# Kernel optimization log

Measured on AMD Instinct MI355X. Metric: run time of the kernel, lower is better.

The kernel has to match this reference:

```python
import jax, jax.numpy as jnp
import numpy as np

B, N, D_IN, D, H = 4, 256, 600, 600, 256  # batch, nodes, in_dim, mem_dim, attn hidden


def setup_inputs() -> dict:
    key = jax.random.key(0)
    ks = jax.random.split(key, 12)
    feature = jax.random.normal(ks[0], (B, N, D_IN), dtype=jnp.float32)
    latent_adj = jax.random.randint(ks[1], (B, N, N), 0, 2).astype(jnp.float32)
    s_in = 1.0 / np.sqrt(D_IN)
    s_d = 1.0 / np.sqrt(D)
    s_2d = 1.0 / np.sqrt(2 * D)
    s_h = 1.0 / np.sqrt(H)
    W0 = jax.random.uniform(ks[2], (D_IN, D), jnp.float32, -s_in, s_in)
    b0 = jax.random.uniform(ks[3], (D,), jnp.float32, -s_in, s_in)
    W1 = jax.random.uniform(ks[4], (D, D), jnp.float32, -s_d, s_d)
    b1 = jax.random.uniform(ks[5], (D,), jnp.float32, -s_d, s_d)
    aW1 = jax.random.uniform(ks[6], (2 * D, H), jnp.float32, -s_2d, s_2d)
    ab1 = jax.random.uniform(ks[7], (H,), jnp.float32, -s_2d, s_2d)
    aW2 = jax.random.uniform(ks[8], (H,), jnp.float32, -s_h, s_h)
    ab2 = jax.random.uniform(ks[9], (1,), jnp.float32, -s_h, s_h)
    return {"feature": feature, "latent_adj": latent_adj, "W0": W0, "b0": b0,
            "W1": W1, "b1": b1, "aW1": aW1, "ab1": ab1, "aW2": aW2, "ab2": ab2}


def _gat_layer(x, Wl, bl, aW1, ab1, aW2, ab2, adj):
    h = jnp.einsum('bni,io->bno', x, Wl) + bl                    # [B,N,D]
    # Decompose first attn linear: [h_i, h_j] @ aW1 = h_i @ aW1[:D] + h_j @ aW1[D:]
    left = jnp.einsum('bnd,dh->bnh', h, aW1[:h.shape[-1]])        # i-part
    right = jnp.einsum('bnd,dh->bnh', h, aW1[h.shape[-1]:])       # j-part
    hid = jax.nn.relu(left[:, :, None, :] + right[:, None, :, :] + ab1)  # [B,N,N,H]
    e = jax.nn.leaky_relu(jnp.einsum('bijh,h->bij', hid, aW2) + ab2[0],
                          negative_slope=0.01)                    # [B,N,N]
    e = jnp.where(adj == 0, jnp.float32(-1e9), e)
    attention = jax.nn.softmax(e, axis=-1) * adj
    return jax.nn.relu(jnp.einsum('bij,bjd->bid', attention, h))


def reference(feature, latent_adj, W0, b0, W1, b1, aW1, ab1, aW2, ab2):
    h = _gat_layer(feature, W0, b0, aW1, ab1, aW2, ab2, latent_adj)
    h = _gat_layer(h, W1, b1, aW1, ab1, aW2, ab2, latent_adj)
    return h
```

## Files before the change

### kernel.cpp

```cpp
#include <hip/hip_runtime.h>
#include <hip/hip_bf16.h>

#define BATCH 4
#define NN    256
#define DD    600
#define HH    256
#define MROWS (BATCH*NN)
#define KPAD  640

typedef __attribute__((ext_vector_type(8))) short bf16x8;
typedef __attribute__((ext_vector_type(4))) float f32x4;

__device__ __forceinline__ void gload16(const void* g, void* l)
{
    __builtin_amdgcn_global_load_lds(
        (const __attribute__((address_space(1))) void*)g,
        (__attribute__((address_space(3))) void*)l, 16, 0, 0);
}

__device__ __forceinline__ void waitcnt_vm(int n)
{
    switch (n) {
    case 0:  asm volatile("s_waitcnt vmcnt(0)"  ::: "memory"); break;
    case 4:  asm volatile("s_waitcnt vmcnt(4)"  ::: "memory"); break;
    case 8:  asm volatile("s_waitcnt vmcnt(8)"  ::: "memory"); break;
    case 12: asm volatile("s_waitcnt vmcnt(12)" ::: "memory"); break;
    default: asm volatile("s_waitcnt vmcnt(0)"  ::: "memory"); break;
    }
}

template<bool BIAS, bool RELU, bool WF32, bool WB16, bool WHT, int NK>
__global__ __launch_bounds__(256) void gemm_mfma(
    const __hip_bfloat16* __restrict__ A, const __hip_bfloat16* __restrict__ BT,
    const float* __restrict__ bias,
    float* __restrict__ Cf, __hip_bfloat16* __restrict__ Cb,
    __hip_bfloat16* __restrict__ hT,
    int lda, int ldb, int ldcf, int ldcb, int Nvalid, int biasN,
    long long sA, long long sBT, long long sCf, long long sCb)
{
    __shared__ __align__(16) char lds[65536];

    const int nwg = gridDim.x * gridDim.y * gridDim.z;
    int lin = blockIdx.x + gridDim.x * (blockIdx.y + gridDim.y * blockIdx.z);
    {
        const int q = nwg >> 3, r = nwg & 7;
        const int xcd = lin & 7, off = lin >> 3;
        lin = (xcd < r ? xcd * (q + 1) : r * (q + 1) + (xcd - r) * q) + off;
    }
    const int bx = lin % gridDim.x;
    const int by = (lin / gridDim.x) % gridDim.y;
    const int bz = lin / (gridDim.x * gridDim.y);

    const int tid  = threadIdx.x;
    const int lane = tid & 63;
    const int wid  = tid >> 6;
    const int wr   = wid >> 1;
    const int wc   = wid & 1;
    const int row0 = by * 64;
    const int col0 = bx * 64;

    const char* Ab = (const char*)A + (bz * sA + (long long)row0 * lda) * 2;
    const char* Bb = (const char*)BT + (bz * sBT + (long long)col0 * ldb) * 2;

    const int sr   = tid >> 3;
    const int scb  = (tid & 7) * 16;
    const int scbs = scb ^ ((sr & 7) << 4);

    const char* gA0 = Ab + (long long)sr        * (lda * 2) + scbs;
    const char* gA1 = Ab + (long long)(sr + 32) * (lda * 2) + scbs;
    const char* gB0 = Bb + (long long)sr        * (ldb * 2) + scbs;
    const char* gB1 = Bb + (long long)(sr + 32) * (ldb * 2) + scbs;

    f32x4 acc[2][2] = {};

    const int fr = lane & 15;
    const int kg = (lane >> 4) * 16;
    const int xv = (fr & 7) << 4;

    auto issue = [&](int t) {
        char* bA = lds + (t & 3) * 8192;
        char* bB = lds + 32768 + (t & 3) * 8192;
        const long long off = (long long)t * 128;
        gload16(gA0 + off, bA + wid * 1024);
        gload16(gA1 + off, bA + 4096 + wid * 1024);
        gload16(gB0 + off, bB + wid * 1024);
        gload16(gB1 + off, bB + 4096 + wid * 1024);
    };

    constexpr int PRE = (NK < 3) ? NK : 3;
    #pragma unroll
    for (int p = 0; p < PRE; ++p) issue(p);

    #pragma unroll
    for (int t = 0; t < NK; ++t) {
        const int imax = (t + 2 < NK - 1) ? t + 2 : NK - 1;
        waitcnt_vm(4 * (imax - t));
        __builtin_amdgcn_s_barrier();
        const char* ldsA = lds + (t & 3) * 8192;
        const char* ldsB = lds + 32768 + (t & 3) * 8192;
        #pragma unroll
        for (int ks = 0; ks < 2; ++ks) {
            const int kb = ks * 64 + kg;
            bf16x8 a0 = *(const bf16x8*)(ldsA + (wr * 32 + fr)      * 128 + (kb ^ xv));
            bf16x8 a1 = *(const bf16x8*)(ldsA + (wr * 32 + 16 + fr) * 128 + (kb ^ xv));
            bf16x8 b0 = *(const bf16x8*)(ldsB + (wc * 32 + fr)      * 128 + (kb ^ xv));
            bf16x8 b1 = *(const bf16x8*)(ldsB + (wc * 32 + 16 + fr) * 128 + (kb ^ xv));
            acc[0][0] = __builtin_amdgcn_mfma_f32_16x16x32_bf16(a0, b0, acc[0][0], 0, 0, 0);
            acc[0][1] = __builtin_amdgcn_mfma_f32_16x16x32_bf16(a0, b1, acc[0][1], 0, 0, 0);
            acc[1][0] = __builtin_amdgcn_mfma_f32_16x16x32_bf16(a1, b0, acc[1][0], 0, 0, 0);
            acc[1][1] = __builtin_amdgcn_mfma_f32_16x16x32_bf16(a1, b1, acc[1][1], 0, 0, 0);
        }
        if (t + 3 < NK) issue(t + 3);
    }
    __syncthreads();

    const int er = (lane >> 4) * 4;
    const int ec = lane & 15;
    __hip_bfloat16* sT = (__hip_bfloat16*)lds;

    #pragma unroll
    for (int mi = 0; mi < 2; ++mi) {
        #pragma unroll
        for (int ni = 0; ni < 2; ++ni) {
            const int lr0 = wr * 32 + mi * 16 + er;
            const int lc  = wc * 32 + ni * 16 + ec;
            const int gr = row0 + lr0;
            const int gc = col0 + lc;
            const float bv = (BIAS && gc < biasN) ? bias[gc] : 0.f;
            #pragma unroll
            for (int r = 0; r < 4; ++r) {
                float v = acc[mi][ni][r] + bv;
                if (RELU) v = fmaxf(v, 0.f);
                const __hip_bfloat16 hv = __float2bfloat16(v);
                const long long row = gr + r;
                if (WF32 && gc < Nvalid)
                    Cf[bz * sCf + row * ldcf + gc] = v;
                if (WB16)
                    Cb[bz * sCb + row * ldcb + gc] = hv;
                if (WHT)
                    sT[(lr0 + r) * 72 + lc] = hv;
            }
        }
    }

    if (WHT) {
        __syncthreads();
        const int b  = row0 >> 8;
        const int i0 = row0 & 255;
        const int cc = tid >> 3;
        const int ch = tid & 7;
        #pragma unroll
        for (int p = 0; p < 2; ++p) {
            const int d = col0 + cc + p * 32;
            __align__(16) __hip_bfloat16 tmp[8];
            #pragma unroll
            for (int u = 0; u < 8; ++u)
                tmp[u] = sT[(ch * 8 + u) * 72 + cc + p * 32];
            *(float4*)&hT[((long long)b * KPAD + d) * NN + i0 + ch * 8] = *(float4*)tmp;
        }
    }
}

__global__ __launch_bounds__(256) void prep_kernel(
    const float* __restrict__ feature, const float* __restrict__ W0,
    const float* __restrict__ W1, const float* __restrict__ aW1,
    __hip_bfloat16* __restrict__ xb, __hip_bfloat16* __restrict__ W0T,
    __hip_bfloat16* __restrict__ W1T, __hip_bfloat16* __restrict__ aW1T)
{
    const int bid = blockIdx.x;
    const int tid = threadIdx.x;
    if (bid < 640) {
        const int idx = (bid * 256 + tid) * 4;
        const int r = idx / KPAD, c = idx % KPAD;
        float4 v = make_float4(0.f, 0.f, 0.f, 0.f);
        if (c < DD) v = *(const float4*)&feature[r * DD + c];
        __align__(8) __hip_bfloat16 o[4] = {
            __float2bfloat16(v.x), __float2bfloat16(v.y),
            __float2bfloat16(v.z), __float2bfloat16(v.w)};
        *(float2*)&xb[idx] = *(float2*)o;
        return;
    }
    __shared__ float tile[32][33];
    const int t = bid - 640;
    const int which = (t < 400) ? 0 : (t < 800) ? 1 : 2;
    const int tt = (which == 0) ? t : (which == 1) ? t - 400 : t - 800;
    const int n0 = (tt / 20) * 32;
    const int k0 = (tt % 20) * 32;
    const int tx = tid & 31, ty = tid >> 5;
    #pragma unroll
    for (int r = 0; r < 4; ++r) {
        const int k = k0 + ty + r * 8;
        const int n = n0 + tx;
        float v = 0.f;
        if (which == 0)      { if (k < DD && n < DD) v = W0[k * DD + n]; }
        else if (which == 1) { if (k < DD && n < DD) v = W1[k * DD + n]; }
        else                 { if (k < DD) v = (n < HH) ? aW1[k * HH + n]
                                                        : aW1[(DD + k) * HH + (n - HH)]; }
        tile[ty + r * 8][tx] = v;
    }
    __syncthreads();
    __hip_bfloat16* dst = (which == 0) ? W0T : (which == 1) ? W1T : aW1T;
    #pragma unroll
    for (int r = 0; r < 4; ++r) {
        const int n = n0 + ty + r * 8;
        const int k = k0 + tx;
        dst[n * KPAD + k] = __float2bfloat16(tile[tx][ty + r * 8]);
    }
}

__device__ __forceinline__ void block_max4(float* v, float (*red)[4])
{
    #pragma unroll
    for (int o = 32; o > 0; o >>= 1)
        #pragma unroll
        for (int q = 0; q < 4; ++q) v[q] = fmaxf(v[q], __shfl_down(v[q], o));
    const int lane = threadIdx.x & 63, w = threadIdx.x >> 6;
    if (lane == 0) { red[w][0]=v[0]; red[w][1]=v[1]; red[w][2]=v[2]; red[w][3]=v[3]; }
    __syncthreads();
    #pragma unroll
    for (int q = 0; q < 4; ++q)
        v[q] = fmaxf(fmaxf(red[0][q], red[1][q]), fmaxf(red[2][q], red[3][q]));
    __syncthreads();
}

__device__ __forceinline__ void block_sum4(float* v, float (*red)[4])
{
    #pragma unroll
    for (int o = 32; o > 0; o >>= 1)
        #pragma unroll
        for (int q = 0; q < 4; ++q) v[q] += __shfl_down(v[q], o);
    const int lane = threadIdx.x & 63, w = threadIdx.x >> 6;
    if (lane == 0) { red[w][0]=v[0]; red[w][1]=v[1]; red[w][2]=v[2]; red[w][3]=v[3]; }
    __syncthreads();
    #pragma unroll
    for (int q = 0; q < 4; ++q)
        v[q] = red[0][q] + red[1][q] + red[2][q] + red[3][q];
    __syncthreads();
}

__global__ __launch_bounds__(256) void attn_kernel(
    const float* __restrict__ LR, const float* __restrict__ aW2,
    const float* __restrict__ ab2, const float* __restrict__ adj,
    __hip_bfloat16* __restrict__ att)
{
    __shared__ float sL[4][HH];
    __shared__ float sW[HH];
    __shared__ float red[4][4];

    const int b  = blockIdx.y;
    const int i0 = blockIdx.x * 4;
    const int j  = threadIdx.x;

    float a[4];
    #pragma unroll
    for (int q = 0; q < 4; ++q)
        a[q] = adj[((long long)(b * NN + i0 + q)) * NN + j];
    const float ab2v = ab2[0];

    sW[j] = aW2[j];
    #pragma unroll
    for (int q = 0; q < 4; ++q)
        sL[q][j] = LR[((long long)(b * NN + i0 + q)) * 512 + j];
    __syncthreads();

    const float* rp = LR + ((long long)(b * NN + j)) * 512 + HH;
    float acc[4] = {0.f, 0.f, 0.f, 0.f};
    for (int h = 0; h < HH; h += 8) {
        const float4 ra = *(const float4*)(rp + h);
        const float4 rb = *(const float4*)(rp + h + 4);
        const float4 w0 = *(const float4*)&sW[h];
        const float4 w1 = *(const float4*)&sW[h + 4];
        #pragma unroll
        for (int q = 0; q < 4; ++q) {
            const float4 l0 = *(const float4*)&sL[q][h];
            const float4 l1 = *(const float4*)&sL[q][h + 4];
            float s = fmaxf(l0.x + ra.x, 0.f) * w0.x;
            s += fmaxf(l0.y + ra.y, 0.f) * w0.y;
            s += fmaxf(l0.z + ra.z, 0.f) * w0.z;
            s += fmaxf(l0.w + ra.w, 0.f) * w0.w;
            s += fmaxf(l1.x + rb.x, 0.f) * w1.x;
            s += fmaxf(l1.y + rb.y, 0.f) * w1.y;
            s += fmaxf(l1.z + rb.z, 0.f) * w1.z;
            s += fmaxf(l1.w + rb.w, 0.f) * w1.w;
            acc[q] += s;
        }
    }

    float m[4];
    #pragma unroll
    for (int q = 0; q < 4; ++q) {
        float e = acc[q] + ab2v;
        e = (e > 0.f) ? e : 0.01f * e;
        m[q] = (a[q] == 0.f) ? -1e9f : e;
    }
    float mx[4] = {m[0], m[1], m[2], m[3]};
    block_max4(mx, red);
    float p[4];
    #pragma unroll
    for (int q = 0; q < 4; ++q) p[q] = __expf(m[q] - mx[q]);
    float s[4] = {p[0], p[1], p[2], p[3]};
    block_sum4(s, red);
    #pragma unroll
    for (int q = 0; q < 4; ++q)
        att[((long long)(b * NN + i0 + q)) * NN + j] = __float2bfloat16(p[q] / s[q] * a[q]);
}

extern "C" void kernel_launch(void* const* d_in, const int* in_sizes, int n_in,
                              void* d_out, int out_size, void* d_ws, size_t ws_size,
                              hipStream_t stream)
{
    const float* feature = (const float*)d_in[0];
    const float* adj     = (const float*)d_in[1];
    const float* W0      = (const float*)d_in[2];
    const float* b0      = (const float*)d_in[3];
    const float* W1      = (const float*)d_in[4];
    const float* b1      = (const float*)d_in[5];
    const float* aW1     = (const float*)d_in[6];
    const float* ab1     = (const float*)d_in[7];
    const float* aW2     = (const float*)d_in[8];
    const float* ab2     = (const float*)d_in[9];
    float* out = (float*)d_out;

    __hip_bfloat16* bw = (__hip_bfloat16*)d_ws;
    __hip_bfloat16* xb   = bw;
    __hip_bfloat16* W0T  = xb   + MROWS * KPAD;
    __hip_bfloat16* W1T  = W0T  + KPAD * KPAD;
    __hip_bfloat16* aW1T = W1T  + KPAD * KPAD;
    __hip_bfloat16* hb   = aW1T + 512 * KPAD;
    __hip_bfloat16* hT   = hb   + MROWS * KPAD;
    __hip_bfloat16* att  = hT   + BATCH * KPAD * NN;
    float* LR = (float*)(att + BATCH * NN * NN);

    prep_kernel<<<1760, 256, 0, stream>>>(feature, W0, W1, aW1, xb, W0T, W1T, aW1T);

    for (int layer = 0; layer < 2; ++layer) {
        const __hip_bfloat16* WT = layer ? W1T : W0T;
        const float* bb          = layer ? b1 : b0;

        gemm_mfma<true, false, false, true, true, KPAD/64><<<dim3(KPAD / 64, MROWS / 64, 1), 256, 0, stream>>>(
            xb, WT, bb, nullptr, hb, hT,
            KPAD, KPAD, 0, KPAD, 0, DD, 0, 0, 0, 0);

        gemm_mfma<true, false, true, false, false, KPAD/64><<<dim3(512 / 64, MROWS / 64, 1), 256, 0, stream>>>(
            hb, aW1T, ab1, LR, nullptr, nullptr,
            KPAD, KPAD, 512, 0, 512, HH, 0, 0, 0, 0);

        attn_kernel<<<dim3(NN / 4, BATCH), 256, 0, stream>>>(LR, aW2, ab2, adj, att);

        if (layer == 0) {
            gemm_mfma<false, true, false, true, false, NN/64><<<dim3(KPAD / 64, NN / 64, BATCH), 256, 0, stream>>>(
                att, hT, nullptr, nullptr, xb, nullptr,
                NN, NN, 0, KPAD, 0, 0,
                (long long)NN * NN, (long long)KPAD * NN, 0, (long long)NN * KPAD);
        } else {
            gemm_mfma<false, true, true, false, false, NN/64><<<dim3(KPAD / 64, NN / 64, BATCH), 256, 0, stream>>>(
                att, hT, nullptr, out, nullptr, nullptr,
                NN, NN, DD, 0, DD, 0,
                (long long)NN * NN, (long long)KPAD * NN, (long long)NN * DD, 0);
        }
    }
}
```

Measured before the change: 67.02 us.

## Fuse fp32-to-bf16 conversion of features and weights into GEMM loaders

Removes the separate prep kernel that converted the feature matrix and transposed and converted W0, W1 and aW1 to bf16. The GEMMs now read fp32 sources directly, convert them in registers and write them swizzled into LDS, using a double-buffered register-staged pipeline for B (and for A in the first layer). This saves one launch and the round trip of the converted copies through global memory. The cost is that conversion and scattered 2-byte LDS writes sit inside every GEMM tile, and each tile re-converts the weights, which the old async global-to-LDS path avoided.

```diff
diff --git a/kernel.cpp b/kernel.cpp
--- a/kernel.cpp
+++ b/kernel.cpp
@@ -22,34 +22,41 @@
 {
     switch (n) {
     case 0:  asm volatile("s_waitcnt vmcnt(0)"  ::: "memory"); break;
+    case 2:  asm volatile("s_waitcnt vmcnt(2)"  ::: "memory"); break;
     case 4:  asm volatile("s_waitcnt vmcnt(4)"  ::: "memory"); break;
+    case 6:  asm volatile("s_waitcnt vmcnt(6)"  ::: "memory"); break;
     case 8:  asm volatile("s_waitcnt vmcnt(8)"  ::: "memory"); break;
-    case 12: asm volatile("s_waitcnt vmcnt(12)" ::: "memory"); break;
     default: asm volatile("s_waitcnt vmcnt(0)"  ::: "memory"); break;
     }
 }
 
-template<bool BIAS, bool RELU, bool WF32, bool WB16, bool WHT, int NK>
-__global__ __launch_bounds__(256) void gemm_mfma(
-    const __hip_bfloat16* __restrict__ A, const __hip_bfloat16* __restrict__ BT,
+__device__ __forceinline__ void lgkm0_barrier()
+{
+    asm volatile("s_waitcnt lgkmcnt(0)" ::: "memory");
+    __builtin_amdgcn_s_barrier();
+}
+
+__device__ __forceinline__ int xcd_remap(int lin, int nwg)
+{
+    const int q = nwg >> 3, r = nwg & 7;
+    const int xcd = lin & 7, off = lin >> 3;
+    return (xcd < r ? xcd * (q + 1) : r * (q + 1) + (xcd - r) * q) + off;
+}
+
+template<bool AF32, bool RELU, bool WF32, bool WB16, bool WHT, bool BPACK, int NK>
+__global__ __launch_bounds__(256) void gemm_cvt(
+    const void* __restrict__ Asrc, const float* __restrict__ Bsrc,
     const float* __restrict__ bias,
     float* __restrict__ Cf, __hip_bfloat16* __restrict__ Cb,
     __hip_bfloat16* __restrict__ hT,
-    int lda, int ldb, int ldcf, int ldcb, int Nvalid, int biasN,
-    long long sA, long long sBT, long long sCf, long long sCb)
-{
-    __shared__ __align__(16) char lds[65536];
-
-    const int nwg = gridDim.x * gridDim.y * gridDim.z;
-    int lin = blockIdx.x + gridDim.x * (blockIdx.y + gridDim.y * blockIdx.z);
-    {
-        const int q = nwg >> 3, r = nwg & 7;
-        const int xcd = lin & 7, off = lin >> 3;
-        lin = (xcd < r ? xcd * (q + 1) : r * (q + 1) + (xcd - r) * q) + off;
-    }
+    int lda, int ldcf, int ldcb, int Nvalid, int biasN)
+{
+    __shared__ __align__(16) char lds[49152];
+
+    const int nwg = gridDim.x * gridDim.y;
+    int lin = xcd_remap(blockIdx.x + gridDim.x * blockIdx.y, nwg);
     const int bx = lin % gridDim.x;
-    const int by = (lin / gridDim.x) % gridDim.y;
-    const int bz = lin / (gridDim.x * gridDim.y);
+    const int by = lin / gridDim.x;
 
     const int tid  = threadIdx.x;
     const int lane = tid & 63;
@@ -59,6 +66,206 @@
     const int row0 = by * 64;
     const int col0 = bx * 64;
 
+    const int bkk = tid >> 4;
+    const int bn4 = (tid & 15) * 4;
+    const int bpr = (BPACK && col0 >= 256) ? 1 : 0;
+    float4 rB[4];
+
+    auto loadB = [&](int t) {
+        const int k0 = t * 64;
+        #pragma unroll
+        for (int p = 0; p < 4; ++p) {
+            const int gk = k0 + bkk + 16 * p;
+            const int gn = col0 + bn4;
+            bool v;
+            const float* src;
+            if (BPACK) {
+                src = Bsrc + ((long long)(gk + 600 * bpr)) * 256 + (gn - 256 * bpr);
+                v = gk < 600;
+            } else {
+                src = Bsrc + (long long)gk * 600 + gn;
+                v = (gk < 600) && (gn < 600);
+            }
+            rB[p] = v ? *(const float4*)src : make_float4(0.f, 0.f, 0.f, 0.f);
+        }
+    };
+    auto writeB = [&](int t) {
+        char* dB = lds + 32768 + (t & 1) * 8192;
+        const int rot = tid & 15;
+        #pragma unroll
+        for (int i = 0; i < 16; ++i) {
+            const int e = (i + rot) & 15;
+            const int p = e >> 2, j = e & 3;
+            const int n = bn4 + j;
+            const int k = bkk + 16 * p;
+            const float* f = (const float*)&rB[p];
+            *(__hip_bfloat16*)(dB + n * 128 + ((2 * k) ^ ((n & 7) << 4))) =
+                __float2bfloat16(f[j]);
+        }
+    };
+
+    const int am16 = tid >> 4;
+    const int ak4  = (tid & 15) * 4;
+    float4 rA[4];
+    auto loadA32 = [&](int t) {
+        const int k0 = t * 64;
+        #pragma unroll
+        for (int p = 0; p < 4; ++p) {
+            const int m  = row0 + am16 + 16 * p;
+            const int gk = k0 + ak4;
+            rA[p] = (gk < 600)
+                ? *(const float4*)((const float*)Asrc + (long long)m * lda + gk)
+                : make_float4(0.f, 0.f, 0.f, 0.f);
+        }
+    };
+    auto writeA32 = [&](int t) {
+        char* dA = lds + (t & 1) * 8192;
+        #pragma unroll
+        for (int p = 0; p < 4; ++p) {
+            const int m = am16 + 16 * p;
+            __align__(8) __hip_bfloat16 o[4] = {
+                __float2bfloat16(rA[p].x), __float2bfloat16(rA[p].y),
+                __float2bfloat16(rA[p].z), __float2bfloat16(rA[p].w)};
+            *(float2*)(dA + m * 128 + ((2 * ak4) ^ ((m & 7) << 4))) = *(float2*)o;
+        }
+    };
+    const int sr   = tid >> 3;
+    const int scb  = (tid & 7) * 16;
+    const int scbs = scb ^ ((sr & 7) << 4);
+    const char* Ab  = (const char*)Asrc + (long long)row0 * lda * 2;
+    const char* gA0 = Ab + (long long)sr        * (lda * 2) + scbs;
+    const char* gA1 = Ab + (long long)(sr + 32) * (lda * 2) + scbs;
+    auto issueA = [&](int t) {
+        char* bA = lds + (t & 3) * 8192;
+        const long long off = (long long)t * 128;
+        gload16(gA0 + off, bA + wid * 1024);
+        gload16(gA1 + off, bA + 4096 + wid * 1024);
+    };
+
+    f32x4 acc[2][2] = {};
+    const int fr = lane & 15;
+    const int kg = (lane >> 4) * 16;
+    const int xv = (fr & 7) << 4;
+
+    auto compute = [&](int t) {
+        const char* lA = lds + (AF32 ? (t & 1) : (t & 3)) * 8192;
+        const char* lB = lds + 32768 + (t & 1) * 8192;
+        #pragma unroll
+        for (int ks = 0; ks < 2; ++ks) {
+            const int kb = ks * 64 + kg;
+            bf16x8 a0 = *(const bf16x8*)(lA + (wr * 32 + fr)      * 128 + (kb ^ xv));
+            bf16x8 a1 = *(const bf16x8*)(lA + (wr * 32 + 16 + fr) * 128 + (kb ^ xv));
+            bf16x8 b0 = *(const bf16x8*)(lB + (wc * 32 + fr)      * 128 + (kb ^ xv));
+            bf16x8 b1 = *(const bf16x8*)(lB + (wc * 32 + 16 + fr) * 128 + (kb ^ xv));
+            acc[0][0] = __builtin_amdgcn_mfma_f32_16x16x32_bf16(a0, b0, acc[0][0], 0, 0, 0);
+            acc[0][1] = __builtin_amdgcn_mfma_f32_16x16x32_bf16(a0, b1, acc[0][1], 0, 0, 0);
+            acc[1][0] = __builtin_amdgcn_mfma_f32_16x16x32_bf16(a1, b0, acc[1][0], 0, 0, 0);
+            acc[1][1] = __builtin_amdgcn_mfma_f32_16x16x32_bf16(a1, b1, acc[1][1], 0, 0, 0);
+        }
+    };
+
+    if constexpr (AF32) {
+        loadA32(0); loadB(0);
+        waitcnt_vm(0);
+        writeA32(0); writeB(0);
+        lgkm0_barrier();
+        #pragma unroll
+        for (int t = 0; t < NK; ++t) {
+            if (t + 1 < NK) { loadA32(t + 1); loadB(t + 1); }
+            compute(t);
+            if (t + 1 < NK) { waitcnt_vm(0); writeA32(t + 1); writeB(t + 1); }
+            lgkm0_barrier();
+        }
+    } else {
+        loadB(0);
+        issueA(0); issueA(1); issueA(2);
+        waitcnt_vm(4);
+        writeB(0);
+        lgkm0_barrier();
+        #pragma unroll
+        for (int t = 0; t < NK; ++t) {
+            if (t + 1 < NK) loadB(t + 1);
+            if (t + 3 < NK) issueA(t + 3);
+            compute(t);
+            if (t + 1 < NK) {
+                waitcnt_vm((t <= NK - 4) ? 2 : 0);
+                writeB(t + 1);
+            }
+            lgkm0_barrier();
+        }
+    }
+    __syncthreads();
+
+    const int er = (lane >> 4) * 4;
+    const int ec = lane & 15;
+    __hip_bfloat16* sT = (__hip_bfloat16*)lds;
+
+    #pragma unroll
+    for (int mi = 0; mi < 2; ++mi) {
+        #pragma unroll
+        for (int ni = 0; ni < 2; ++ni) {
+            const int lr0 = wr * 32 + mi * 16 + er;
+            const int lc  = wc * 32 + ni * 16 + ec;
+            const int gr = row0 + lr0;
+            const int gc = col0 + lc;
+            const float bv = (bias != nullptr && gc < biasN) ? bias[gc] : 0.f;
+            #pragma unroll
+            for (int r = 0; r < 4; ++r) {
+                float v = acc[mi][ni][r] + bv;
+                if (RELU) v = fmaxf(v, 0.f);
+                const __hip_bfloat16 hv = __float2bfloat16(v);
+                const long long row = gr + r;
+                if (WF32 && gc < Nvalid)
+                    Cf[row * ldcf + gc] = v;
+                if (WB16)
+                    Cb[row * ldcb + gc] = hv;
+                if (WHT)
+                    sT[(lr0 + r) * 72 + lc] = hv;
+            }
+        }
+    }
+
+    if (WHT) {
+        __syncthreads();
+        const int b  = row0 >> 8;
+        const int i0 = row0 & 255;
+        const int cc = tid >> 3;
+        const int ch = tid & 7;
+        #pragma unroll
+        for (int p = 0; p < 2; ++p) {
+            const int d = col0 + cc + p * 32;
+            __align__(16) __hip_bfloat16 tmp[8];
+            #pragma unroll
+            for (int u = 0; u < 8; ++u)
+                tmp[u] = sT[(ch * 8 + u) * 72 + cc + p * 32];
+            *(float4*)&hT[((long long)b * KPAD + d) * NN + i0 + ch * 8] = *(float4*)tmp;
+        }
+    }
+}
+
+template<bool RELU, bool WF32, bool WB16, int NK>
+__global__ __launch_bounds__(256) void gemm_mfma(
+    const __hip_bfloat16* __restrict__ A, const __hip_bfloat16* __restrict__ BT,
+    float* __restrict__ Cf, __hip_bfloat16* __restrict__ Cb,
+    int lda, int ldb, int ldcf, int ldcb, int Nvalid,
+    long long sA, long long sBT, long long sCf, long long sCb)
+{
+    __shared__ __align__(16) char lds[65536];
+
+    const int nwg = gridDim.x * gridDim.y * gridDim.z;
+    int lin = xcd_remap(blockIdx.x + gridDim.x * (blockIdx.y + gridDim.y * blockIdx.z), nwg);
+    const int bx = lin % gridDim.x;
+    const int by = (lin / gridDim.x) % gridDim.y;
+    const int bz = lin / (gridDim.x * gridDim.y);
+
+    const int tid  = threadIdx.x;
+    const int lane = tid & 63;
+    const int wid  = tid >> 6;
+    const int wr   = wid >> 1;
+    const int wc   = wid & 1;
+    const int row0 = by * 64;
+    const int col0 = bx * 64;
+
     const char* Ab = (const char*)A + (bz * sA + (long long)row0 * lda) * 2;
     const char* Bb = (const char*)BT + (bz * sBT + (long long)col0 * ldb) * 2;
 
@@ -72,7 +279,6 @@
     const char* gB1 = Bb + (long long)(sr + 32) * (ldb * 2) + scbs;
 
     f32x4 acc[2][2] = {};
-
     const int fr = lane & 15;
     const int kg = (lane >> 4) * 16;
     const int xv = (fr & 7) << 4;
@@ -96,15 +302,15 @@
         const int imax = (t + 2 < NK - 1) ? t + 2 : NK - 1;
         waitcnt_vm(4 * (imax - t));
         __builtin_amdgcn_s_barrier();
-        const char* ldsA = lds + (t & 3) * 8192;
-        const char* ldsB = lds + 32768 + (t & 3) * 8192;
+        const char* lA = lds + (t & 3) * 8192;
+        const char* lB = lds + 32768 + (t & 3) * 8192;
         #pragma unroll
         for (int ks = 0; ks < 2; ++ks) {
             const int kb = ks * 64 + kg;
-            bf16x8 a0 = *(const bf16x8*)(ldsA + (wr * 32 + fr)      * 128 + (kb ^ xv));
-            bf16x8 a1 = *(const bf16x8*)(ldsA + (wr * 32 + 16 + fr) * 128 + (kb ^ xv));
-            bf16x8 b0 = *(const bf16x8*)(ldsB + (wc * 32 + fr)      * 128 + (kb ^ xv));
-            bf16x8 b1 = *(const bf16x8*)(ldsB + (wc * 32 + 16 + fr) * 128 + (kb ^ xv));
+            bf16x8 a0 = *(const bf16x8*)(lA + (wr * 32 + fr)      * 128 + (kb ^ xv));
+            bf16x8 a1 = *(const bf16x8*)(lA + (wr * 32 + 16 + fr) * 128 + (kb ^ xv));
+            bf16x8 b0 = *(const bf16x8*)(lB + (wc * 32 + fr)      * 128 + (kb ^ xv));
+            bf16x8 b1 = *(const bf16x8*)(lB + (wc * 32 + 16 + fr) * 128 + (kb ^ xv));
             acc[0][0] = __builtin_amdgcn_mfma_f32_16x16x32_bf16(a0, b0, acc[0][0], 0, 0, 0);
             acc[0][1] = __builtin_amdgcn_mfma_f32_16x16x32_bf16(a0, b1, acc[0][1], 0, 0, 0);
             acc[1][0] = __builtin_amdgcn_mfma_f32_16x16x32_bf16(a1, b0, acc[1][0], 0, 0, 0);
@@ -116,95 +322,23 @@
 
     const int er = (lane >> 4) * 4;
     const int ec = lane & 15;
-    __hip_bfloat16* sT = (__hip_bfloat16*)lds;
-
     #pragma unroll
     for (int mi = 0; mi < 2; ++mi) {
         #pragma unroll
         for (int ni = 0; ni < 2; ++ni) {
-            const int lr0 = wr * 32 + mi * 16 + er;
-            const int lc  = wc * 32 + ni * 16 + ec;
-            const int gr = row0 + lr0;
-            const int gc = col0 + lc;
-            const float bv = (BIAS && gc < biasN) ? bias[gc] : 0.f;
+            const int gr = row0 + wr * 32 + mi * 16 + er;
+            const int gc = col0 + wc * 32 + ni * 16 + ec;
             #pragma unroll
             for (int r = 0; r < 4; ++r) {
-                float v = acc[mi][ni][r] + bv;
+                float v = acc[mi][ni][r];
                 if (RELU) v = fmaxf(v, 0.f);
-                const __hip_bfloat16 hv = __float2bfloat16(v);
                 const long long row = gr + r;
                 if (WF32 && gc < Nvalid)
                     Cf[bz * sCf + row * ldcf + gc] = v;
                 if (WB16)
-                    Cb[bz * sCb + row * ldcb + gc] = hv;
-                if (WHT)
-                    sT[(lr0 + r) * 72 + lc] = hv;
+                    Cb[bz * sCb + row * ldcb + gc] = __float2bfloat16(v);
             }
         }
-    }
-
-    if (WHT) {
-        __syncthreads();
-        const int b  = row0 >> 8;
-        const int i0 = row0 & 255;
-        const int cc = tid >> 3;
-        const int ch = tid & 7;
-        #pragma unroll
-        for (int p = 0; p < 2; ++p) {
-            const int d = col0 + cc + p * 32;
-            __align__(16) __hip_bfloat16 tmp[8];
-            #pragma unroll
-            for (int u = 0; u < 8; ++u)
-                tmp[u] = sT[(ch * 8 + u) * 72 + cc + p * 32];
-            *(float4*)&hT[((long long)b * KPAD + d) * NN + i0 + ch * 8] = *(float4*)tmp;
-        }
-    }
-}
-
-__global__ __launch_bounds__(256) void prep_kernel(
-    const float* __restrict__ feature, const float* __restrict__ W0,
-    const float* __restrict__ W1, const float* __restrict__ aW1,
-    __hip_bfloat16* __restrict__ xb, __hip_bfloat16* __restrict__ W0T,
-    __hip_bfloat16* __restrict__ W1T, __hip_bfloat16* __restrict__ aW1T)
-{
-    const int bid = blockIdx.x;
-    const int tid = threadIdx.x;
-    if (bid < 640) {
-        const int idx = (bid * 256 + tid) * 4;
-        const int r = idx / KPAD, c = idx % KPAD;
-        float4 v = make_float4(0.f, 0.f, 0.f, 0.f);
-        if (c < DD) v = *(const float4*)&feature[r * DD + c];
-        __align__(8) __hip_bfloat16 o[4] = {
-            __float2bfloat16(v.x), __float2bfloat16(v.y),
-            __float2bfloat16(v.z), __float2bfloat16(v.w)};
-        *(float2*)&xb[idx] = *(float2*)o;
-        return;
-    }
-    __shared__ float tile[32][33];
-    const int t = bid - 640;
-    const int which = (t < 400) ? 0 : (t < 800) ? 1 : 2;
-    const int tt = (which == 0) ? t : (which == 1) ? t - 400 : t - 800;
-    const int n0 = (tt / 20) * 32;
-    const int k0 = (tt % 20) * 32;
-    const int tx = tid & 31, ty = tid >> 5;
-    #pragma unroll
-    for (int r = 0; r < 4; ++r) {
-        const int k = k0 + ty + r * 8;
-        const int n = n0 + tx;
-        float v = 0.f;
-        if (which == 0)      { if (k < DD && n < DD) v = W0[k * DD + n]; }
-        else if (which == 1) { if (k < DD && n < DD) v = W1[k * DD + n]; }
-        else                 { if (k < DD) v = (n < HH) ? aW1[k * HH + n]
-                                                        : aW1[(DD + k) * HH + (n - HH)]; }
-        tile[ty + r * 8][tx] = v;
-    }
-    __syncthreads();
-    __hip_bfloat16* dst = (which == 0) ? W0T : (which == 1) ? W1T : aW1T;
-    #pragma unroll
-    for (int r = 0; r < 4; ++r) {
-        const int n = n0 + ty + r * 8;
-        const int k = k0 + tx;
-        dst[n * KPAD + k] = __float2bfloat16(tile[tx][ty + r * 8]);
     }
 }
 
@@ -322,40 +456,46 @@
     float* out = (float*)d_out;
 
     __hip_bfloat16* bw = (__hip_bfloat16*)d_ws;
-    __hip_bfloat16* xb   = bw;
-    __hip_bfloat16* W0T  = xb   + MROWS * KPAD;
-    __hip_bfloat16* W1T  = W0T  + KPAD * KPAD;
-    __hip_bfloat16* aW1T = W1T  + KPAD * KPAD;
-    __hip_bfloat16* hb   = aW1T + 512 * KPAD;
-    __hip_bfloat16* hT   = hb   + MROWS * KPAD;
-    __hip_bfloat16* att  = hT   + BATCH * KPAD * NN;
+    __hip_bfloat16* xb  = bw;
+    __hip_bfloat16* hb  = xb + MROWS * KPAD;
+    __hip_bfloat16* hT  = hb + MROWS * KPAD;
+    __hip_bfloat16* att = hT + BATCH * KPAD * NN;
     float* LR = (float*)(att + BATCH * NN * NN);
 
-    prep_kernel<<<1760, 256, 0, stream>>>(feature, W0, W1, aW1, xb, W0T, W1T, aW1T);
-
     for (int layer = 0; layer < 2; ++layer) {
-        const __hip_bfloat16* WT = layer ? W1T : W0T;
-        const float* bb          = layer ? b1 : b0;
-
-        gemm_mfma<true, false, false, true, true, KPAD/64><<<dim3(KPAD / 64, MROWS / 64, 1), 256, 0, stream>>>(
-            xb, WT, bb, nullptr, hb, hT,
-            KPAD, KPAD, 0, KPAD, 0, DD, 0, 0, 0, 0);
-
-        gemm_mfma<true, false, true, false, false, KPAD/64><<<dim3(512 / 64, MROWS / 64, 1), 256, 0, stream>>>(
-            hb, aW1T, ab1, LR, nullptr, nullptr,
-            KPAD, KPAD, 512, 0, 512, HH, 0, 0, 0, 0);
+        const float* W  = layer ? W1 : W0;
+        const float* bb = layer ? b1 : b0;
+
+        if (layer == 0) {
+            gemm_cvt<true, false, false, true, true, false, KPAD/64>
+                <<<dim3(KPAD / 64, MROWS / 64), 256, 0, stream>>>(
+                feature, W, bb, nullptr, hb, hT,
+                DD, 0, KPAD, 0, DD);
+        } else {
+            gemm_cvt<false, false, false, true, true, false, KPAD/64>
+                <<<dim3(KPAD / 64, MROWS / 64), 256, 0, stream>>>(
+                xb, W, bb, nullptr, hb, hT,
+                KPAD, 0, KPAD, 0, DD);
+        }
+
+        gemm_cvt<false, false, true, false, false, true, KPAD/64>
+            <<<dim3(512 / 64, MROWS / 64), 256, 0, stream>>>(
+            hb, aW1, ab1, LR, nullptr, nullptr,
+            KPAD, 512, 0, 512, HH);
 
         attn_kernel<<<dim3(NN / 4, BATCH), 256, 0, stream>>>(LR, aW2, ab2, adj, att);
 
         if (layer == 0) {
-            gemm_mfma<false, true, false, true, false, NN/64><<<dim3(KPAD / 64, NN / 64, BATCH), 256, 0, stream>>>(
-                att, hT, nullptr, nullptr, xb, nullptr,
-                NN, NN, 0, KPAD, 0, 0,
+            gemm_mfma<true, false, true, NN/64>
+                <<<dim3(KPAD / 64, NN / 64, BATCH), 256, 0, stream>>>(
+                att, hT, nullptr, xb,
+                NN, NN, 0, KPAD, 0,
                 (long long)NN * NN, (long long)KPAD * NN, 0, (long long)NN * KPAD);
         } else {
-            gemm_mfma<false, true, true, false, false, NN/64><<<dim3(KPAD / 64, NN / 64, BATCH), 256, 0, stream>>>(
-                att, hT, nullptr, out, nullptr, nullptr,
-                NN, NN, DD, 0, DD, 0,
+            gemm_mfma<true, true, false, NN/64>
+                <<<dim3(KPAD / 64, NN / 64, BATCH), 256, 0, stream>>>(
+                att, hT, out, nullptr,
+                NN, NN, DD, 0, DD,
                 (long long)NN * NN, (long long)KPAD * NN, (long long)NN * DD, 0);
         }
     }
```

Result: slower. 144.2 us (+115.1%).

## Fold attention projection into node linear via precomputed combined weights

Applied to the files above, without the earlier changes.

Precomputes W·aW1 (and bias·aW1) so that one fused GEMM per layer produces h, the left attention projection and a transposed right projection at once. This removes the dependent second GEMM launch per layer. The attention kernel now reads the right projection in transposed layout, which gives coalesced per-j loads. The cost is an extra weight-product GEMM and more prep work each call, plus some precision change from composing the weights in bf16.

```diff
diff --git a/kernel.cpp b/kernel.cpp
--- a/kernel.cpp
+++ b/kernel.cpp
@@ -7,6 +7,7 @@
 #define HH    256
 #define MROWS (BATCH*NN)
 #define KPAD  640
+#define NFUSE 1152
 
 typedef __attribute__((ext_vector_type(8))) short bf16x8;
 typedef __attribute__((ext_vector_type(4))) float f32x4;
@@ -24,29 +25,30 @@
     case 0:  asm volatile("s_waitcnt vmcnt(0)"  ::: "memory"); break;
     case 4:  asm volatile("s_waitcnt vmcnt(4)"  ::: "memory"); break;
     case 8:  asm volatile("s_waitcnt vmcnt(8)"  ::: "memory"); break;
-    case 12: asm volatile("s_waitcnt vmcnt(12)" ::: "memory"); break;
     default: asm volatile("s_waitcnt vmcnt(0)"  ::: "memory"); break;
     }
 }
 
-template<bool BIAS, bool RELU, bool WF32, bool WB16, bool WHT, int NK>
+__device__ __forceinline__ int xcd_remap(int lin, int nwg)
+{
+    const int q = nwg >> 3, r = nwg & 7;
+    const int xcd = lin & 7, off = lin >> 3;
+    return (xcd < r ? xcd * (q + 1) : r * (q + 1) + (xcd - r) * q) + off;
+}
+
+template<bool BIAS, bool RELU, bool WF32, bool WB16, bool WHT, bool FUSEDLR, int NK>
 __global__ __launch_bounds__(256) void gemm_mfma(
     const __hip_bfloat16* __restrict__ A, const __hip_bfloat16* __restrict__ BT,
     const float* __restrict__ bias,
     float* __restrict__ Cf, __hip_bfloat16* __restrict__ Cb,
-    __hip_bfloat16* __restrict__ hT,
+    __hip_bfloat16* __restrict__ hT, float* __restrict__ RT,
     int lda, int ldb, int ldcf, int ldcb, int Nvalid, int biasN,
     long long sA, long long sBT, long long sCf, long long sCb)
 {
     __shared__ __align__(16) char lds[65536];
 
     const int nwg = gridDim.x * gridDim.y * gridDim.z;
-    int lin = blockIdx.x + gridDim.x * (blockIdx.y + gridDim.y * blockIdx.z);
-    {
-        const int q = nwg >> 3, r = nwg & 7;
-        const int xcd = lin & 7, off = lin >> 3;
-        lin = (xcd < r ? xcd * (q + 1) : r * (q + 1) + (xcd - r) * q) + off;
-    }
+    int lin = xcd_remap(blockIdx.x + gridDim.x * (blockIdx.y + gridDim.y * blockIdx.z), nwg);
     const int bx = lin % gridDim.x;
     const int by = (lin / gridDim.x) % gridDim.y;
     const int bz = lin / (gridDim.x * gridDim.y);
@@ -72,7 +74,6 @@
     const char* gB1 = Bb + (long long)(sr + 32) * (ldb * 2) + scbs;
 
     f32x4 acc[2][2] = {};
-
     const int fr = lane & 15;
     const int kg = (lane >> 4) * 16;
     const int xv = (fr & 7) << 4;
@@ -96,15 +97,15 @@
         const int imax = (t + 2 < NK - 1) ? t + 2 : NK - 1;
         waitcnt_vm(4 * (imax - t));
         __builtin_amdgcn_s_barrier();
-        const char* ldsA = lds + (t & 3) * 8192;
-        const char* ldsB = lds + 32768 + (t & 3) * 8192;
+        const char* lA = lds + (t & 3) * 8192;
+        const char* lB = lds + 32768 + (t & 3) * 8192;
         #pragma unroll
         for (int ks = 0; ks < 2; ++ks) {
             const int kb = ks * 64 + kg;
-            bf16x8 a0 = *(const bf16x8*)(ldsA + (wr * 32 + fr)      * 128 + (kb ^ xv));
-            bf16x8 a1 = *(const bf16x8*)(ldsA + (wr * 32 + 16 + fr) * 128 + (kb ^ xv));
-            bf16x8 b0 = *(const bf16x8*)(ldsB + (wc * 32 + fr)      * 128 + (kb ^ xv));
-            bf16x8 b1 = *(const bf16x8*)(ldsB + (wc * 32 + 16 + fr) * 128 + (kb ^ xv));
+            bf16x8 a0 = *(const bf16x8*)(lA + (wr * 32 + fr)      * 128 + (kb ^ xv));
+            bf16x8 a1 = *(const bf16x8*)(lA + (wr * 32 + 16 + fr) * 128 + (kb ^ xv));
+            bf16x8 b0 = *(const bf16x8*)(lB + (wc * 32 + fr)      * 128 + (kb ^ xv));
+            bf16x8 b1 = *(const bf16x8*)(lB + (wc * 32 + 16 + fr) * 128 + (kb ^ xv));
             acc[0][0] = __builtin_amdgcn_mfma_f32_16x16x32_bf16(a0, b0, acc[0][0], 0, 0, 0);
             acc[0][1] = __builtin_amdgcn_mfma_f32_16x16x32_bf16(a0, b1, acc[0][1], 0, 0, 0);
             acc[1][0] = __builtin_amdgcn_mfma_f32_16x16x32_bf16(a1, b0, acc[1][0], 0, 0, 0);
@@ -118,45 +119,107 @@
     const int ec = lane & 15;
     __hip_bfloat16* sT = (__hip_bfloat16*)lds;
 
-    #pragma unroll
-    for (int mi = 0; mi < 2; ++mi) {
-        #pragma unroll
-        for (int ni = 0; ni < 2; ++ni) {
-            const int lr0 = wr * 32 + mi * 16 + er;
-            const int lc  = wc * 32 + ni * 16 + ec;
-            const int gr = row0 + lr0;
-            const int gc = col0 + lc;
-            const float bv = (BIAS && gc < biasN) ? bias[gc] : 0.f;
-            #pragma unroll
-            for (int r = 0; r < 4; ++r) {
-                float v = acc[mi][ni][r] + bv;
-                if (RELU) v = fmaxf(v, 0.f);
-                const __hip_bfloat16 hv = __float2bfloat16(v);
-                const long long row = gr + r;
-                if (WF32 && gc < Nvalid)
-                    Cf[bz * sCf + row * ldcf + gc] = v;
-                if (WB16)
-                    Cb[bz * sCb + row * ldcb + gc] = hv;
-                if (WHT)
-                    sT[(lr0 + r) * 72 + lc] = hv;
-            }
-        }
-    }
-
-    if (WHT) {
-        __syncthreads();
-        const int b  = row0 >> 8;
-        const int i0 = row0 & 255;
-        const int cc = tid >> 3;
-        const int ch = tid & 7;
-        #pragma unroll
-        for (int p = 0; p < 2; ++p) {
-            const int d = col0 + cc + p * 32;
-            __align__(16) __hip_bfloat16 tmp[8];
-            #pragma unroll
-            for (int u = 0; u < 8; ++u)
-                tmp[u] = sT[(ch * 8 + u) * 72 + cc + p * 32];
-            *(float4*)&hT[((long long)b * KPAD + d) * NN + i0 + ch * 8] = *(float4*)tmp;
+    if constexpr (FUSEDLR) {
+        if (col0 >= 896) {
+            #pragma unroll
+            for (int mi = 0; mi < 2; ++mi) {
+                #pragma unroll
+                for (int ni = 0; ni < 2; ++ni) {
+                    const int gr = row0 + wr * 32 + mi * 16 + er;
+                    const int gc = col0 + wc * 32 + ni * 16 + ec;
+                    const float bv = bias[gc];
+                    f32x4 q = acc[mi][ni];
+                    float4 o = make_float4(q[0] + bv, q[1] + bv, q[2] + bv, q[3] + bv);
+                    const int b = gr >> 8, j = gr & 255;
+                    *(float4*)&RT[((long long)(b * 256 + (gc - 896))) * 256 + j] = o;
+                }
+            }
+        } else if (col0 >= 640) {
+            #pragma unroll
+            for (int mi = 0; mi < 2; ++mi) {
+                #pragma unroll
+                for (int ni = 0; ni < 2; ++ni) {
+                    const int gr = row0 + wr * 32 + mi * 16 + er;
+                    const int gc = col0 + wc * 32 + ni * 16 + ec;
+                    const float bv = bias[gc];
+                    #pragma unroll
+                    for (int r = 0; r < 4; ++r)
+                        Cf[(long long)(gr + r) * ldcf + (gc - 640)] = acc[mi][ni][r] + bv;
+                }
+            }
+        } else {
+            #pragma unroll
+            for (int mi = 0; mi < 2; ++mi) {
+                #pragma unroll
+                for (int ni = 0; ni < 2; ++ni) {
+                    const int lr0 = wr * 32 + mi * 16 + er;
+                    const int lc  = wc * 32 + ni * 16 + ec;
+                    const int gr = row0 + lr0;
+                    const int gc = col0 + lc;
+                    const float bv = bias[gc];
+                    #pragma unroll
+                    for (int r = 0; r < 4; ++r) {
+                        const __hip_bfloat16 hv = __float2bfloat16(acc[mi][ni][r] + bv);
+                        Cb[(long long)(gr + r) * ldcb + gc] = hv;
+                        sT[(lr0 + r) * 72 + lc] = hv;
+                    }
+                }
+            }
+            __syncthreads();
+            const int b  = row0 >> 8;
+            const int i0 = row0 & 255;
+            const int cc = tid >> 3;
+            const int ch = tid & 7;
+            #pragma unroll
+            for (int p = 0; p < 2; ++p) {
+                const int d = col0 + cc + p * 32;
+                __align__(16) __hip_bfloat16 tmp[8];
+                #pragma unroll
+                for (int u = 0; u < 8; ++u)
+                    tmp[u] = sT[(ch * 8 + u) * 72 + cc + p * 32];
+                *(float4*)&hT[((long long)b * KPAD + d) * NN + i0 + ch * 8] = *(float4*)tmp;
+            }
+        }
+    } else {
+        #pragma unroll
+        for (int mi = 0; mi < 2; ++mi) {
+            #pragma unroll
+            for (int ni = 0; ni < 2; ++ni) {
+                const int lr0 = wr * 32 + mi * 16 + er;
+                const int lc  = wc * 32 + ni * 16 + ec;
+                const int gr = row0 + lr0;
+                const int gc = col0 + lc;
+                const float bv = (BIAS && gc < biasN) ? bias[gc] : 0.f;
+                #pragma unroll
+                for (int r = 0; r < 4; ++r) {
+                    float v = acc[mi][ni][r] + bv;
+                    if (RELU) v = fmaxf(v, 0.f);
+                    const __hip_bfloat16 hv = __float2bfloat16(v);
+                    const long long row = gr + r;
+                    if (WF32 && gc < Nvalid)
+                        Cf[bz * sCf + row * ldcf + gc] = v;
+                    if (WB16)
+                        Cb[bz * sCb + row * ldcb + gc] = hv;
+                    if (WHT)
+                        sT[(lr0 + r) * 72 + lc] = hv;
+                }
+            }
+        }
+        if (WHT) {
+            __syncthreads();
+            const int b  = row0 >> 8;
+            const int i0 = row0 & 255;
+            const int cc = tid >> 3;
+            const int ch = tid & 7;
+            #pragma unroll
+            for (int p = 0; p < 2; ++p) {
+                const int d = col0 + cc + p * 32;
+                __align__(16) __hip_bfloat16 tmp[8];
+                #pragma unroll
+                for (int u = 0; u < 8; ++u)
+                    tmp[u] = sT[(ch * 8 + u) * 72 + cc + p * 32];
+                *(float4*)&hT[((long long)b * KPAD + d) * NN + i0 + ch * 8] = *(float4*)tmp;
+            }
         }
     }
 }
@@ -164,13 +227,17 @@
 __global__ __launch_bounds__(256) void prep_kernel(
     const float* __restrict__ feature, const float* __restrict__ W0,
     const float* __restrict__ W1, const float* __restrict__ aW1,
-    __hip_bfloat16* __restrict__ xb, __hip_bfloat16* __restrict__ W0T,
-    __hip_bfloat16* __restrict__ W1T, __hip_bfloat16* __restrict__ aW1T)
-{
-    const int bid = blockIdx.x;
+    const float* __restrict__ b0, const float* __restrict__ b1,
+    const float* __restrict__ ab1,
+    __hip_bfloat16* __restrict__ xb, __hip_bfloat16* __restrict__ UT,
+    __hip_bfloat16* __restrict__ aW1T, __hip_bfloat16* __restrict__ Wb,
+    float* __restrict__ fb)
+{
+    const int u   = blockIdx.x;
     const int tid = threadIdx.x;
-    if (bid < 640) {
-        const int idx = (bid * 256 + tid) * 4;
+
+    if (u < 640) {
+        const int idx = (u * 256 + tid) * 4;
         const int r = idx / KPAD, c = idx % KPAD;
         float4 v = make_float4(0.f, 0.f, 0.f, 0.f);
         if (c < DD) v = *(const float4*)&feature[r * DD + c];
@@ -180,31 +247,67 @@
         *(float2*)&xb[idx] = *(float2*)o;
         return;
     }
-    __shared__ float tile[32][33];
-    const int t = bid - 640;
-    const int which = (t < 400) ? 0 : (t < 800) ? 1 : 2;
-    const int tt = (which == 0) ? t : (which == 1) ? t - 400 : t - 800;
-    const int n0 = (tt / 20) * 32;
-    const int k0 = (tt % 20) * 32;
-    const int tx = tid & 31, ty = tid >> 5;
-    #pragma unroll
-    for (int r = 0; r < 4; ++r) {
-        const int k = k0 + ty + r * 8;
-        const int n = n0 + tx;
-        float v = 0.f;
-        if (which == 0)      { if (k < DD && n < DD) v = W0[k * DD + n]; }
-        else if (which == 1) { if (k < DD && n < DD) v = W1[k * DD + n]; }
-        else                 { if (k < DD) v = (n < HH) ? aW1[k * HH + n]
-                                                        : aW1[(DD + k) * HH + (n - HH)]; }
-        tile[ty + r * 8][tx] = v;
-    }
-    __syncthreads();
-    __hip_bfloat16* dst = (which == 0) ? W0T : (which == 1) ? W1T : aW1T;
-    #pragma unroll
-    for (int r = 0; r < 4; ++r) {
-        const int n = n0 + ty + r * 8;
-        const int k = k0 + tx;
-        dst[n * KPAD + k] = __float2bfloat16(tile[tx][ty + r * 8]);
+    if (u < 1760) {
+        __shared__ float tile[32][33];
+        const int t = u - 640;
+        const int which = (t < 400) ? 0 : (t < 800) ? 1 : 2;
+        const int tt = (which == 0) ? t : (which == 1) ? t - 400 : t - 800;
+        const int n0 = (tt / 20) * 32;
+        const int k0 = (tt % 20) * 32;
+        const int tx = tid & 31, ty = tid >> 5;
+        #pragma unroll
+        for (int r = 0; r < 4; ++r) {
+            const int k = k0 + ty + r * 8;
+            const int n = n0 + tx;
+            float v = 0.f;
+            if (which == 0)      { if (k < DD && n < DD) v = W0[k * DD + n]; }
+            else if (which == 1) { if (k < DD && n < DD) v = W1[k * DD + n]; }
+            else                 { if (k < DD) v = (n < HH) ? aW1[k * HH + n]
+                                                            : aW1[(DD + k) * HH + (n - HH)]; }
+            tile[ty + r * 8][tx] = v;
+        }
+        __syncthreads();
+        __hip_bfloat16* dst = (which == 0) ? UT
+                            : (which == 1) ? UT + (long long)NFUSE * KPAD
+                            : aW1T;
+        #pragma unroll
+        for (int r = 0; r < 4; ++r) {
+            const int n = n0 + ty + r * 8;
+            const int k = k0 + tx;
+            dst[(long long)n * KPAD + k] = __float2bfloat16(tile[tx][ty + r * 8]);
+        }
+        return;
+    }
+    if (u < 2560) {
+        const int t = u - 1760;
+        const int which = (t < 400) ? 0 : 1;
+        const int tt = which ? t - 400 : t;
+        const float* W = which ? W1 : W0;
+        const int idx = (tt * 256 + tid) * 4;
+        const int i = idx / KPAD, o = idx % KPAD;
+        float4 v = make_float4(0.f, 0.f, 0.f, 0.f);
+        if (i < DD && o < DD) v = *(const float4*)&W[i * DD + o];
+        __align__(8) __hip_bfloat16 ob[4] = {
+            __float2bfloat16(v.x), __float2bfloat16(v.y),
+            __float2bfloat16(v.z), __float2bfloat16(v.w)};
+        *(float2*)&Wb[(long long)which * KPAD * KPAD + idx] = *(float2*)ob;
+        return;
+    }
+    if (u < 2564) {
+        const int idx = u - 2560;
+        const int l = idx >> 1, p = idx & 1;
+        const float* bl = l ? b1 : b0;
+        float acc = 0.f;
+        for (int d = 0; d < DD; ++d)
+            acc += bl[d] * aW1[(long long)(d + DD * p) * HH + tid];
+        fb[l * NFUSE + 640 + p * 256 + tid] = acc + (p == 0 ? ab1[tid] : 0.f);
+        return;
+    }
+    {
+        const int e = (u - 2564) * 256 + tid;
+        const int l = e / 640, c = e % 640;
+        const float* bl = l ? b1 : b0;
+        fb[l * NFUSE + c] = (c < DD) ? bl[c] : 0.f;
     }
 }
 
@@ -239,9 +342,9 @@
 }
 
 __global__ __launch_bounds__(256) void attn_kernel(
-    const float* __restrict__ LR, const float* __restrict__ aW2,
-    const float* __restrict__ ab2, const float* __restrict__ adj,
-    __hip_bfloat16* __restrict__ att)
+    const float* __restrict__ LRL, const float* __restrict__ RT,
+    const float* __restrict__ aW2, const float* __restrict__ ab2,
+    const float* __restrict__ adj, __hip_bfloat16* __restrict__ att)
 {
     __shared__ float sL[4][HH];
     __shared__ float sW[HH];
@@ -260,28 +363,29 @@
     sW[j] = aW2[j];
     #pragma unroll
     for (int q = 0; q < 4; ++q)
-        sL[q][j] = LR[((long long)(b * NN + i0 + q)) * 512 + j];
-    __syncthreads();
-
-    const float* rp = LR + ((long long)(b * NN + j)) * 512 + HH;
+        sL[q][j] = LRL[((long long)(b * NN + i0 + q)) * HH + j];
+    __syncthreads();
+
+    const float* rp = RT + (long long)b * HH * NN + j;
     float acc[4] = {0.f, 0.f, 0.f, 0.f};
     for (int h = 0; h < HH; h += 8) {
-        const float4 ra = *(const float4*)(rp + h);
-        const float4 rb = *(const float4*)(rp + h + 4);
+        float rv[8];
+        #pragma unroll
+        for (int u = 0; u < 8; ++u) rv[u] = rp[(h + u) * NN];
         const float4 w0 = *(const float4*)&sW[h];
         const float4 w1 = *(const float4*)&sW[h + 4];
         #pragma unroll
         for (int q = 0; q < 4; ++q) {
             const float4 l0 = *(const float4*)&sL[q][h];
             const float4 l1 = *(const float4*)&sL[q][h + 4];
-            float s = fmaxf(l0.x + ra.x, 0.f) * w0.x;
-            s += fmaxf(l0.y + ra.y, 0.f) * w0.y;
-            s += fmaxf(l0.z + ra.z, 0.f) * w0.z;
-            s += fmaxf(l0.w + ra.w, 0.f) * w0.w;
-            s += fmaxf(l1.x + rb.x, 0.f) * w1.x;
-            s += fmaxf(l1.y + rb.y, 0.f) * w1.y;
-            s += fmaxf(l1.z + rb.z, 0.f) * w1.z;
-            s += fmaxf(l1.w + rb.w, 0.f) * w1.w;
+            float s = fmaxf(l0.x + rv[0], 0.f) * w0.x;
+            s += fmaxf(l0.y + rv[1], 0.f) * w0.y;
+            s += fmaxf(l0.z + rv[2], 0.f) * w0.z;
+            s += fmaxf(l0.w + rv[3], 0.f) * w0.w;
+            s += fmaxf(l1.x + rv[4], 0.f) * w1.x;
+            s += fmaxf(l1.y + rv[5], 0.f) * w1.y;
+            s += fmaxf(l1.z + rv[6], 0.f) * w1.z;
+            s += fmaxf(l1.w + rv[7], 0.f) * w1.w;
             acc[q] += s;
         }
     }
@@ -321,40 +425,46 @@
     const float* ab2     = (const float*)d_in[9];
     float* out = (float*)d_out;
 
+    const long long UTsz = (long long)NFUSE * KPAD;
     __hip_bfloat16* bw = (__hip_bfloat16*)d_ws;
     __hip_bfloat16* xb   = bw;
-    __hip_bfloat16* W0T  = xb   + MROWS * KPAD;
-    __hip_bfloat16* W1T  = W0T  + KPAD * KPAD;
-    __hip_bfloat16* aW1T = W1T  + KPAD * KPAD;
-    __hip_bfloat16* hb   = aW1T + 512 * KPAD;
+    __hip_bfloat16* UT   = xb   + MROWS * KPAD;
+    __hip_bfloat16* aW1T = UT   + 2 * UTsz;
+    __hip_bfloat16* Wb   = aW1T + 512 * KPAD;
+    __hip_bfloat16* hb   = Wb   + 2 * KPAD * KPAD;
     __hip_bfloat16* hT   = hb   + MROWS * KPAD;
     __hip_bfloat16* att  = hT   + BATCH * KPAD * NN;
-    float* LR = (float*)(att + BATCH * NN * NN);
-
-    prep_kernel<<<1760, 256, 0, stream>>>(feature, W0, W1, aW1, xb, W0T, W1T, aW1T);
+    float* LRL = (float*)(att + BATCH * NN * NN);
+    float* RT  = LRL + MROWS * HH;
+    float* fb  = RT  + BATCH * HH * NN;
+
+    prep_kernel<<<2569, 256, 0, stream>>>(
+        feature, W0, W1, aW1, b0, b1, ab1, xb, UT, aW1T, Wb, fb);
+
+    gemm_mfma<false, false, false, true, false, false, KPAD/64>
+        <<<dim3(KPAD / 64, 512 / 64, 2), 256, 0, stream>>>(
+        aW1T, Wb, nullptr, nullptr, UT + (long long)KPAD * KPAD, nullptr, nullptr,
+        KPAD, KPAD, 0, KPAD, 0, 0,
+        0, (long long)KPAD * KPAD, 0, UTsz);
 
     for (int layer = 0; layer < 2; ++layer) {
-        const __hip_bfloat16* WT = layer ? W1T : W0T;
-        const float* bb          = layer ? b1 : b0;
-
-        gemm_mfma<true, false, false, true, true, KPAD/64><<<dim3(KPAD / 64, MROWS / 64, 1), 256, 0, stream>>>(
-            xb, WT, bb, nullptr, hb, hT,
-            KPAD, KPAD, 0, KPAD, 0, DD, 0, 0, 0, 0);
-
-        gemm_mfma<true, false, true, false, false, KPAD/64><<<dim3(512 / 64, MROWS / 64, 1), 256, 0, stream>>>(
-            hb, aW1T, ab1, LR, nullptr, nullptr,
-            KPAD, KPAD, 512, 0, 512, HH, 0, 0, 0, 0);
-
-        attn_kernel<<<dim3(NN / 4, BATCH), 256, 0, stream>>>(LR, aW2, ab2, adj, att);
+        gemm_mfma<true, false, false, false, false, true, KPAD/64>
+            <<<dim3(NFUSE / 64, MROWS / 64, 1), 256, 0, stream>>>(
+            xb, UT + layer * UTsz, fb + layer * NFUSE, LRL, hb, hT, RT,
+            KPAD, KPAD, HH, KPAD, 0, NFUSE, 0, 0, 0, 0);
+
+        attn_kernel<<<dim3(NN / 4, BATCH), 256, 0, stream>>>(LRL, RT, aW2, ab2, adj, att);
 
         if (layer == 0) {
-            gemm_mfma<false, true, false, true, false, NN/64><<<dim3(KPAD / 64, NN / 64, BATCH), 256, 0, stream>>>(
-                att, hT, nullptr, nullptr, xb, nullptr,
+            gemm_mfma<false, true, false, true, false, false, NN/64>
+                <<<dim3(KPAD / 64, NN / 64, BATCH), 256, 0, stream>>>(
+                att, hT, nullptr, nullptr, xb, nullptr, nullptr,
                 NN, NN, 0, KPAD, 0, 0,
                 (long long)NN * NN, (long long)KPAD * NN, 0, (long long)NN * KPAD);
         } else {
-            gemm_mfma<false, true, true, false, false, NN/64><<<dim3(KPAD / 64, NN / 64, BATCH), 256, 0, stream>>>(
-                att, hT, nullptr, out, nullptr, nullptr,
+            gemm_mfma<false, true, true, false, false, false, NN/64>
+                <<<dim3(KPAD / 64, NN / 64, BATCH), 256, 0, stream>>>(
+                att, hT, nullptr, out, nullptr, nullptr, nullptr,
                 NN, NN, DD, 0, DD, 0,
                 (long long)NN * NN, (long long)KPAD * NN, (long long)NN * DD, 0);
         }
```

After: 85.65 us. +27.8%, slower.
